# Performance work log

Hardware: AMD Instinct MI355X
Metric: run time of the kernel (lower is better)

The kernel has to match this reference:

```python
import jax, jax.numpy as jnp
import numpy as np

N, E = 50000, 800000
IN_C, HID, OUT_C, HEADS = 256, 32, 16, 8
NEG_SLOPE = 0.2


def gat_conv(x, edge_index, W, att_src, att_dst, bias, heads, out_c, concat):
    """PyG-style GATConv (inference, dropout off, add_self_loops=True).

    x: [N, F_in], edge_index: [2, E] with row0=src(j), row1=dst(i).
    W: [F_in, heads*out_c], att_src/att_dst: [heads, out_c], bias: [heads*out_c] or [out_c].
    """
    n = x.shape[0]
    loops = jnp.arange(n, dtype=edge_index.dtype)
    src = jnp.concatenate([edge_index[0], loops])
    dst = jnp.concatenate([edge_index[1], loops])

    xl = (x @ W).reshape(n, heads, out_c)              # [N, H, C]
    a_src = jnp.einsum('nhc,hc->nh', xl, att_src)      # [N, H]
    a_dst = jnp.einsum('nhc,hc->nh', xl, att_dst)

    e = a_src[src] + a_dst[dst]                        # [E', H]
    e = jnp.where(e >= 0, e, NEG_SLOPE * e)            # leaky_relu
    e_max = jax.ops.segment_max(e, dst, num_segments=n)
    e_exp = jnp.exp(e - e_max[dst])
    denom = jax.ops.segment_sum(e_exp, dst, num_segments=n)
    alpha = e_exp / (denom[dst] + 1e-16)               # segment softmax over in-edges of dst

    msg = alpha[:, :, None] * xl[src]                  # [E', H, C]
    out = jax.ops.segment_sum(msg, dst, num_segments=n)  # [N, H, C]
    if concat:
        out = out.reshape(n, heads * out_c)
    else:
        out = out.mean(axis=1)
    return out + bias


def setup_inputs() -> dict:
    key = jax.random.key(0)
    ks = jax.random.split(key, 10)
    s_in = 1.0 / np.sqrt(IN_C)
    s_h = 1.0 / np.sqrt(HEADS * HID)
    x = jax.random.normal(ks[0], (N, IN_C), dtype=jnp.float32)
    edge_index = jax.random.randint(ks[1], (2, E), 0, N, dtype=jnp.int64)
    return {
        'x': x,
        'edge_index': edge_index,
        'W1': jax.random.normal(ks[2], (IN_C, HEADS * HID), dtype=jnp.float32) * s_in,
        'att_src1': jax.random.normal(ks[3], (HEADS, HID), dtype=jnp.float32) * s_h,
        'att_dst1': jax.random.normal(ks[4], (HEADS, HID), dtype=jnp.float32) * s_h,
        'b1': jnp.zeros((HEADS * HID,), dtype=jnp.float32),
        'W2': jax.random.normal(ks[5], (HEADS * HID, OUT_C), dtype=jnp.float32) * s_h,
        'att_src2': jax.random.normal(ks[6], (1, OUT_C), dtype=jnp.float32) * 0.1,
        'att_dst2': jax.random.normal(ks[7], (1, OUT_C), dtype=jnp.float32) * 0.1,
        'b2': jnp.zeros((OUT_C,), dtype=jnp.float32),
    }


def reference(x, edge_index, W1, att_src1, att_dst1, b1, W2, att_src2, att_dst2, b2):
    h = gat_conv(x, edge_index, W1, att_src1, att_dst1, b1, HEADS, HID, concat=True)
    h = jax.nn.relu(h)
    # F.dropout(training=False) is identity at inference
    out = gat_conv(h, edge_index, W2, att_src2, att_dst2, b2, 1, OUT_C, concat=False)
    return jax.nn.log_softmax(out, axis=1)
```

## Files before the change

kernel.cpp:

```cpp
#include <hip/hip_runtime.h>

#define IN_C 256
#define H1 8
#define C1 32
#define F1 256
#define OC 16
#define NEG 0.2f

typedef short short8 __attribute__((ext_vector_type(8)));
typedef unsigned short ushort8 __attribute__((ext_vector_type(8)));
typedef float floatx4 __attribute__((ext_vector_type(4)));

__device__ __forceinline__ unsigned short f2bf(float f) {
    unsigned u = __builtin_bit_cast(unsigned, f);
    u = (u + 0x7fffu + ((u >> 16) & 1u)) >> 16;
    return (unsigned short)u;
}
__device__ __forceinline__ float bf2f(unsigned short h) {
    unsigned u = ((unsigned)h) << 16;
    return __builtin_bit_cast(float, u);
}

__global__ __launch_bounds__(256) void k_fuse0(const int* __restrict__ ei,
                                               int* __restrict__ cnt,
                                               const float* __restrict__ W1,
                                               const float* __restrict__ W2,
                                               unsigned short* __restrict__ w1t,
                                               unsigned short* __restrict__ w2t, int E)
{
    int gid = blockIdx.x * 256 + threadIdx.x;
    if (gid < E) atomicAdd(&cnt[ei[E + gid]], 1);
    if (gid < 65536) {
        int n = gid >> 8, k = gid & 255;
        w1t[n * 256 + k] = f2bf(W1[k * 256 + n]);
    } else if (gid < 65536 + 4096) {
        int r = gid - 65536;
        int n = r >> 8, k = r & 255;
        w2t[n * 256 + k] = f2bf(W2[k * 16 + n]);
    }
}

__global__ __launch_bounds__(256) void k_gemm1(const float* __restrict__ A,
                                               const unsigned short* __restrict__ Bt,
                                               const float* __restrict__ att_s,
                                               const float* __restrict__ att_d,
                                               unsigned short* __restrict__ Cb,
                                               float* __restrict__ asrc,
                                               float* __restrict__ adst, int M)
{
    __shared__ short As[128][40];
    __shared__ short Bs[128][40];
    const int tid  = threadIdx.x;
    const int lane = tid & 63;
    const int w    = tid >> 6;
    const int bm   = blockIdx.x * 128;
    const int bn   = blockIdx.y * 128;
    const int wm   = (w >> 1) * 64;
    const int wn   = (w & 1) * 64;
    const int srow = tid >> 1;
    const int soff = (tid & 1) * 16;
    floatx4 acc[4][4] = {};
    for (int k0 = 0; k0 < 256; k0 += 32) {
        __syncthreads();
        {
            int gr = bm + srow;
            float4 f0 = {0,0,0,0}, f1 = {0,0,0,0}, f2 = {0,0,0,0}, f3 = {0,0,0,0};
            if (gr < M) {
                const float4* p = (const float4*)(A + (size_t)gr * 256 + k0 + soff);
                f0 = p[0]; f1 = p[1]; f2 = p[2]; f3 = p[3];
            }
            ushort8 v0, v1;
            v0[0]=f2bf(f0.x); v0[1]=f2bf(f0.y); v0[2]=f2bf(f0.z); v0[3]=f2bf(f0.w);
            v0[4]=f2bf(f1.x); v0[5]=f2bf(f1.y); v0[6]=f2bf(f1.z); v0[7]=f2bf(f1.w);
            v1[0]=f2bf(f2.x); v1[1]=f2bf(f2.y); v1[2]=f2bf(f2.z); v1[3]=f2bf(f2.w);
            v1[4]=f2bf(f3.x); v1[5]=f2bf(f3.y); v1[6]=f2bf(f3.z); v1[7]=f2bf(f3.w);
            *(ushort8*)&As[srow][soff]     = v0;
            *(ushort8*)&As[srow][soff + 8] = v1;
        }
        {
            const ushort8* p = (const ushort8*)(Bt + (size_t)(bn + srow) * 256 + k0 + soff);
            *(ushort8*)&Bs[srow][soff]     = p[0];
            *(ushort8*)&Bs[srow][soff + 8] = p[1];
        }
        __syncthreads();
        short8 af[4], bf[4];
        const int q8 = (lane >> 4) * 8;
        const int l15i = lane & 15;
#pragma unroll
        for (int i = 0; i < 4; ++i) af[i] = *(const short8*)&As[wm + i * 16 + l15i][q8];
#pragma unroll
        for (int j = 0; j < 4; ++j) bf[j] = *(const short8*)&Bs[wn + j * 16 + l15i][q8];
#pragma unroll
        for (int i = 0; i < 4; ++i)
#pragma unroll
            for (int j = 0; j < 4; ++j)
                acc[i][j] = __builtin_amdgcn_mfma_f32_16x16x32_bf16(af[i], bf[j], acc[i][j], 0, 0, 0);
    }
    const int l15 = lane & 15;
    const int rq  = (lane >> 4) * 4;
    const int hA = (bn + wn) >> 5;
    const int hB = hA + 1;
    const float aS_A0 = att_s[hA * 32 + l15],      aS_A1 = att_s[hA * 32 + 16 + l15];
    const float aS_B0 = att_s[hB * 32 + l15],      aS_B1 = att_s[hB * 32 + 16 + l15];
    const float aD_A0 = att_d[hA * 32 + l15],      aD_A1 = att_d[hA * 32 + 16 + l15];
    const float aD_B0 = att_d[hB * 32 + l15],      aD_B1 = att_d[hB * 32 + 16 + l15];
#pragma unroll
    for (int i = 0; i < 4; ++i) {
#pragma unroll
        for (int reg = 0; reg < 4; ++reg) {
            int gr = bm + wm + i * 16 + rq + reg;
            float sA = acc[i][0][reg] * aS_A0 + acc[i][1][reg] * aS_A1;
            float dA = acc[i][0][reg] * aD_A0 + acc[i][1][reg] * aD_A1;
            float sB = acc[i][2][reg] * aS_B0 + acc[i][3][reg] * aS_B1;
            float dB = acc[i][2][reg] * aD_B0 + acc[i][3][reg] * aD_B1;
#pragma unroll
            for (int o = 1; o < 16; o <<= 1) {
                sA += __shfl_xor(sA, o, 16);  dA += __shfl_xor(dA, o, 16);
                sB += __shfl_xor(sB, o, 16);  dB += __shfl_xor(dB, o, 16);
            }
            if (gr < M) {
#pragma unroll
                for (int j = 0; j < 4; ++j)
                    Cb[(size_t)gr * 256 + bn + wn + j * 16 + l15] = f2bf(acc[i][j][reg]);
                if (l15 == 0) {
                    asrc[(size_t)gr * H1 + hA] = sA;  adst[(size_t)gr * H1 + hA] = dA;
                    asrc[(size_t)gr * H1 + hB] = sB;  adst[(size_t)gr * H1 + hB] = dB;
                }
            }
        }
    }
}

__global__ __launch_bounds__(256) void k_scan_a(const int* __restrict__ cnt,
                                                int* __restrict__ rp,
                                                int* __restrict__ bsum, int N)
{
    __shared__ int ws4[4];
    int t = threadIdx.x, lane = t & 63, wid = t >> 6;
    int i = blockIdx.x * 256 + t;
    int v = (i < N) ? cnt[i] : 0;
    int incl = v;
#pragma unroll
    for (int off = 1; off < 64; off <<= 1) {
        int tv = __shfl_up(incl, off, 64);
        if (lane >= off) incl += tv;
    }
    if (lane == 63) ws4[wid] = incl;
    __syncthreads();
    int add = 0;
    for (int w = 0; w < wid; ++w) add += ws4[w];
    incl += add;
    if (i < N) rp[i + 1] = incl;
    if (t == 255) bsum[blockIdx.x] = incl;
}

__global__ __launch_bounds__(256) void k_scan_b(const int* __restrict__ bsum,
                                                int* __restrict__ boff, int NB)
{
    __shared__ int ws4[4];
    int t = threadIdx.x, lane = t & 63, wid = t >> 6;
    int i0 = t * 4;
    int v[4];
#pragma unroll
    for (int k = 0; k < 4; ++k) { int i = i0 + k; v[k] = (i < NB) ? bsum[i] : 0; }
    int s = v[0] + v[1] + v[2] + v[3];
    int incl = s;
#pragma unroll
    for (int off = 1; off < 64; off <<= 1) {
        int tv = __shfl_up(incl, off, 64);
        if (lane >= off) incl += tv;
    }
    if (lane == 63) ws4[wid] = incl;
    __syncthreads();
    int wpre = 0;
    for (int w = 0; w < wid; ++w) wpre += ws4[w];
    int run = wpre + incl - s;
#pragma unroll
    for (int k = 0; k < 4; ++k) {
        int i = i0 + k;
        if (i < NB) boff[i] = run;
        run += v[k];
    }
}

__global__ __launch_bounds__(256) void k_scan_c(int* __restrict__ rp,
                                                const int* __restrict__ boff,
                                                const int* __restrict__ cnt,
                                                int* __restrict__ cur, int N)
{
    int i = blockIdx.x * 256 + threadIdx.x;
    if (i < N) {
        int v = rp[i + 1] + boff[blockIdx.x];
        rp[i + 1] = v;
        cur[i] = v - cnt[i];
    }
    if (i == 0) rp[0] = 0;
}

__global__ __launch_bounds__(256) void k_scatter(const int* __restrict__ ei,
                                                 int* __restrict__ cur,
                                                 int* __restrict__ ssrc, int E)
{
    int e = blockIdx.x * 256 + threadIdx.x;
    if (e >= E) return;
    int s = ei[e];
    int d = ei[E + e];
    int pos = atomicAdd(&cur[d], 1);
    ssrc[pos] = s;
}

__global__ __launch_bounds__(256) void k_gather1(const int* __restrict__ rp,
                                                 const int* __restrict__ ssrc,
                                                 const unsigned short* __restrict__ xl,
                                                 const float* __restrict__ asrc,
                                                 const float* __restrict__ adst,
                                                 const float* __restrict__ bias,
                                                 unsigned short* __restrict__ hout, int N)
{
    int lane = threadIdx.x & 63;
    int node = blockIdx.x * 4 + (threadIdx.x >> 6);
    if (node >= N) return;
    int half = lane >> 5;
    int l31  = lane & 31;
    int c8   = l31 * 8;
    int h    = l31 >> 2;
    float ad = adst[(size_t)node * H1 + h];

    float4 a0 = {0,0,0,0}, a1 = {0,0,0,0};
    float den = 0.f;

    if (half == 0) {
        float e = asrc[(size_t)node * H1 + h] + ad;
        e = e >= 0.f ? e : NEG * e;
        float w = __expf(e);
        ushort8 r = *(const ushort8*)(xl + (size_t)node * F1 + c8);
        a0.x += w*bf2f(r[0]); a0.y += w*bf2f(r[1]); a0.z += w*bf2f(r[2]); a0.w += w*bf2f(r[3]);
        a1.x += w*bf2f(r[4]); a1.y += w*bf2f(r[5]); a1.z += w*bf2f(r[6]); a1.w += w*bf2f(r[7]);
        den += w;
    }

    int jb = rp[node];
    int Ecnt = rp[node + 1] - jb;
    int k = half;
    for (; k + 2 < Ecnt; k += 4) {
        int s0 = ssrc[jb + k];
        int s1 = ssrc[jb + k + 2];
        float e0 = asrc[(size_t)s0 * H1 + h] + ad;
        float e1 = asrc[(size_t)s1 * H1 + h] + ad;
        ushort8 r0 = *(const ushort8*)(xl + (size_t)s0 * F1 + c8);
        ushort8 r1 = *(const ushort8*)(xl + (size_t)s1 * F1 + c8);
        e0 = e0 >= 0.f ? e0 : NEG * e0;  float w0 = __expf(e0);
        e1 = e1 >= 0.f ? e1 : NEG * e1;  float w1 = __expf(e1);
        den += w0 + w1;
        a0.x += w0*bf2f(r0[0]) + w1*bf2f(r1[0]);
        a0.y += w0*bf2f(r0[1]) + w1*bf2f(r1[1]);
        a0.z += w0*bf2f(r0[2]) + w1*bf2f(r1[2]);
        a0.w += w0*bf2f(r0[3]) + w1*bf2f(r1[3]);
        a1.x += w0*bf2f(r0[4]) + w1*bf2f(r1[4]);
        a1.y += w0*bf2f(r0[5]) + w1*bf2f(r1[5]);
        a1.z += w0*bf2f(r0[6]) + w1*bf2f(r1[6]);
        a1.w += w0*bf2f(r0[7]) + w1*bf2f(r1[7]);
    }
    if (k < Ecnt) {
        int s = ssrc[jb + k];
        float e = asrc[(size_t)s * H1 + h] + ad;
        e = e >= 0.f ? e : NEG * e;
        float w = __expf(e);
        ushort8 r = *(const ushort8*)(xl + (size_t)s * F1 + c8);
        den += w;
        a0.x += w*bf2f(r[0]); a0.y += w*bf2f(r[1]); a0.z += w*bf2f(r[2]); a0.w += w*bf2f(r[3]);
        a1.x += w*bf2f(r[4]); a1.y += w*bf2f(r[5]); a1.z += w*bf2f(r[6]); a1.w += w*bf2f(r[7]);
    }
    a0.x += __shfl_xor(a0.x, 32);  a0.y += __shfl_xor(a0.y, 32);
    a0.z += __shfl_xor(a0.z, 32);  a0.w += __shfl_xor(a0.w, 32);
    a1.x += __shfl_xor(a1.x, 32);  a1.y += __shfl_xor(a1.y, 32);
    a1.z += __shfl_xor(a1.z, 32);  a1.w += __shfl_xor(a1.w, 32);
    den  += __shfl_xor(den, 32);
    if (half == 0) {
        float inv = 1.f / (den + 1e-16f);
        const float4* bv = (const float4*)(bias + c8);
        float4 b0 = bv[0], b1 = bv[1];
        ushort8 o;
        o[0] = f2bf(fmaxf(a0.x * inv + b0.x, 0.f));
        o[1] = f2bf(fmaxf(a0.y * inv + b0.y, 0.f));
        o[2] = f2bf(fmaxf(a0.z * inv + b0.z, 0.f));
        o[3] = f2bf(fmaxf(a0.w * inv + b0.w, 0.f));
        o[4] = f2bf(fmaxf(a1.x * inv + b1.x, 0.f));
        o[5] = f2bf(fmaxf(a1.y * inv + b1.y, 0.f));
        o[6] = f2bf(fmaxf(a1.z * inv + b1.z, 0.f));
        o[7] = f2bf(fmaxf(a1.w * inv + b1.w, 0.f));
        *(ushort8*)(hout + (size_t)node * F1 + c8) = o;
    }
}

__global__ __launch_bounds__(256) void k_gemm2(const unsigned short* __restrict__ Hm,
                                               const unsigned short* __restrict__ W2t,
                                               const float* __restrict__ as2,
                                               const float* __restrict__ ad2,
                                               unsigned short* __restrict__ xl2b,
                                               float* __restrict__ asrc,
                                               float* __restrict__ adst, int N)
{
    const int lane = threadIdx.x & 63;
    const int wid  = threadIdx.x >> 6;
    const int rowbase = blockIdx.x * 64 + wid * 16;
    const int col = lane & 15;
    const int q8  = (lane >> 4) * 8;
    const int m   = rowbase + col;
    const bool mv = m < N;
    const unsigned short* arow = Hm + (size_t)m * 256 + q8;
    const unsigned short* brow = W2t + (size_t)col * 256 + q8;
    floatx4 acc = {0.f, 0.f, 0.f, 0.f};
#pragma unroll
    for (int t = 0; t < 8; ++t) {
        short8 af = {0,0,0,0,0,0,0,0};
        if (mv) af = *(const short8*)(arow + t * 32);
        short8 bf = *(const short8*)(brow + t * 32);
        acc = __builtin_amdgcn_mfma_f32_16x16x32_bf16(af, bf, acc, 0, 0, 0);
    }
    float s_as = as2[col], s_ad = ad2[col];
    const int rq = (lane >> 4) * 4;
#pragma unroll
    for (int reg = 0; reg < 4; ++reg) {
        int row = rowbase + rq + reg;
        float v = acc[reg];
        float s1 = v * s_as, s2 = v * s_ad;
#pragma unroll
        for (int o = 1; o < 16; o <<= 1) { s1 += __shfl_xor(s1, o, 16); s2 += __shfl_xor(s2, o, 16); }
        if (row < N) {
            xl2b[(size_t)row * OC + col] = f2bf(v);
            if (col == 0) { asrc[row] = s1; adst[row] = s2; }
        }
    }
}

__global__ __launch_bounds__(256) void k_gather2(const int* __restrict__ rp,
                                                 const int* __restrict__ ssrc,
                                                 const unsigned short* __restrict__ xl2b,
                                                 const float* __restrict__ asrc,
                                                 const float* __restrict__ adst,
                                                 const float* __restrict__ bias,
                                                 float* __restrict__ out, int N)
{
    int sub  = threadIdx.x & 15;
    int node = blockIdx.x * 16 + (threadIdx.x >> 4);
    if (node >= N) return;
    float ad = adst[node];
    float e = asrc[node] + ad;
    e = e >= 0.f ? e : NEG * e;
    float w = __expf(e);
    float acc = w * bf2f(xl2b[(size_t)node * OC + sub]);
    float den = w;
    int jb = rp[node], je = rp[node + 1];
    int j = jb;
    for (; j + 4 <= je; j += 4) {
        int s0 = ssrc[j], s1i = ssrc[j+1], s2i = ssrc[j+2], s3i = ssrc[j+3];
        float e0 = asrc[s0] + ad, e1 = asrc[s1i] + ad, e2 = asrc[s2i] + ad, e3 = asrc[s3i] + ad;
        float v0 = bf2f(xl2b[(size_t)s0 * OC + sub]);
        float v1 = bf2f(xl2b[(size_t)s1i * OC + sub]);
        float v2 = bf2f(xl2b[(size_t)s2i * OC + sub]);
        float v3 = bf2f(xl2b[(size_t)s3i * OC + sub]);
        e0 = e0 >= 0.f ? e0 : NEG * e0;  float w0 = __expf(e0);
        e1 = e1 >= 0.f ? e1 : NEG * e1;  float w1 = __expf(e1);
        e2 = e2 >= 0.f ? e2 : NEG * e2;  float w2 = __expf(e2);
        e3 = e3 >= 0.f ? e3 : NEG * e3;  float w3 = __expf(e3);
        den += w0 + w1 + w2 + w3;
        acc += w0 * v0 + w1 * v1 + w2 * v2 + w3 * v3;
    }
    for (; j < je; ++j) {
        int s = ssrc[j];
        float ev = asrc[s] + ad;
        ev = ev >= 0.f ? ev : NEG * ev;
        float wv = __expf(ev);
        acc += wv * bf2f(xl2b[(size_t)s * OC + sub]);
        den += wv;
    }
    float v = acc / (den + 1e-16f) + bias[sub];
    float m = v;
#pragma unroll
    for (int o = 1; o < 16; o <<= 1) m = fmaxf(m, __shfl_xor(m, o, 16));
    float ex = __expf(v - m);
    float ss = ex;
#pragma unroll
    for (int o = 1; o < 16; o <<= 1) ss += __shfl_xor(ss, o, 16);
    out[(size_t)node * OC + sub] = v - m - logf(ss);
}

extern "C" void kernel_launch(void* const* d_in, const int* in_sizes, int n_in,
                              void* d_out, int out_size, void* d_ws, size_t ws_size,
                              hipStream_t stream)
{
    const float* x   = (const float*)d_in[0];
    const int*   ei  = (const int*)d_in[1];
    const float* W1  = (const float*)d_in[2];
    const float* as1 = (const float*)d_in[3];
    const float* ad1 = (const float*)d_in[4];
    const float* b1  = (const float*)d_in[5];
    const float* W2  = (const float*)d_in[6];
    const float* as2 = (const float*)d_in[7];
    const float* ad2 = (const float*)d_in[8];
    const float* b2  = (const float*)d_in[9];
    float* out = (float*)d_out;

    const int N = in_sizes[0] / IN_C;
    const int E = in_sizes[1] / 2;
    const int NB = (N + 255) / 256;

    char* base = (char*)d_ws;
    unsigned short* xl1b = (unsigned short*)base;
    unsigned short* hb   = xl1b + (size_t)N * F1;
    unsigned short* w1t  = hb + (size_t)N * F1;
    unsigned short* w2t  = w1t + 256 * 256;
    unsigned short* xl2b = w2t + 16 * 256;
    float* asrc1 = (float*)(xl2b + (size_t)N * OC);
    float* adst1 = asrc1 + (size_t)N * H1;
    float* asrc2 = adst1 + (size_t)N * H1;
    float* adst2 = asrc2 + N;
    int*   rp    = (int*)(adst2 + N);
    int*   cnt   = rp + (N + 1);
    int*   cur   = cnt + N;
    int*   bsum  = cur + N;
    int*   boff  = bsum + 1024;
    int*   ssrc  = boff + 1024;

    hipMemsetAsync(cnt, 0, (size_t)N * sizeof(int), stream);
    k_fuse0<<<(E + 255) / 256, 256, 0, stream>>>(ei, cnt, W1, W2, w1t, w2t, E);
    k_scan_a<<<NB, 256, 0, stream>>>(cnt, rp, bsum, N);
    k_scan_b<<<1, 256, 0, stream>>>(bsum, boff, NB);
    k_scan_c<<<NB, 256, 0, stream>>>(rp, boff, cnt, cur, N);
    k_scatter<<<(E + 255) / 256, 256, 0, stream>>>(ei, cur, ssrc, E);

    k_gemm1<<<dim3((N + 127) / 128, 2), 256, 0, stream>>>(x, w1t, as1, ad1, xl1b, asrc1, adst1, N);
    k_gather1<<<(N + 3) / 4, 256, 0, stream>>>(rp, ssrc, xl1b, asrc1, adst1, b1, hb, N);

    k_gemm2<<<(N + 63) / 64, 256, 0, stream>>>(hb, w2t, as2, ad2, xl2b, asrc2, adst2, N);
    k_gather2<<<(N + 15) / 16, 256, 0, stream>>>(rp, ssrc, xl2b, asrc2, adst2, b2, out, N);
}
```

Measured before the change: 322.4 us.

## Fuse CSR build into one cooperative kernel and widen gemm1 to full output width

```diff
diff --git a/kernel.cpp b/kernel.cpp
--- a/kernel.cpp
+++ b/kernel.cpp
@@ -1,4 +1,7 @@
 #include <hip/hip_runtime.h>
+#include <hip/hip_cooperative_groups.h>
+
+namespace cg = cooperative_groups;
 
 #define IN_C 256
 #define H1 8
@@ -21,22 +24,90 @@
     return __builtin_bit_cast(float, u);
 }
 
-__global__ __launch_bounds__(256) void k_fuse0(const int* __restrict__ ei,
-                                               int* __restrict__ cnt,
-                                               const float* __restrict__ W1,
-                                               const float* __restrict__ W2,
-                                               unsigned short* __restrict__ w1t,
-                                               unsigned short* __restrict__ w2t, int E)
-{
-    int gid = blockIdx.x * 256 + threadIdx.x;
-    if (gid < E) atomicAdd(&cnt[ei[E + gid]], 1);
-    if (gid < 65536) {
-        int n = gid >> 8, k = gid & 255;
+__global__ __launch_bounds__(256) void k_csr(const int* __restrict__ ei,
+                                             const float* __restrict__ W1,
+                                             const float* __restrict__ W2,
+                                             unsigned short* __restrict__ w1t,
+                                             unsigned short* __restrict__ w2t,
+                                             int* __restrict__ cnt,
+                                             int* __restrict__ rp,
+                                             int* __restrict__ cur,
+                                             int* __restrict__ bsum,
+                                             int* __restrict__ boff,
+                                             int* __restrict__ ssrc,
+                                             int N, int E)
+{
+    cg::grid_group grid = cg::this_grid();
+    __shared__ int ws4[4];
+    const int tid  = threadIdx.x;
+    const int lane = tid & 63;
+    const int wid  = tid >> 6;
+    const int b    = blockIdx.x;
+    const int gt   = b * 256 + tid;
+    const int GT   = gridDim.x * 256;
+
+    for (int i = gt; i < N; i += GT) cnt[i] = 0;
+    {
+        int n = gt >> 8, k = gt & 255;
         w1t[n * 256 + k] = f2bf(W1[k * 256 + n]);
-    } else if (gid < 65536 + 4096) {
-        int r = gid - 65536;
-        int n = r >> 8, k = r & 255;
+    }
+    if (gt < 4096) {
+        int n = gt >> 8, k = gt & 255;
         w2t[n * 256 + k] = f2bf(W2[k * 16 + n]);
+    }
+    grid.sync();
+
+    for (int e = gt; e < E; e += GT) atomicAdd(&cnt[ei[E + e]], 1);
+    grid.sync();
+
+    {
+        int v = (gt < N) ? cnt[gt] : 0;
+        int incl = v;
+#pragma unroll
+        for (int off = 1; off < 64; off <<= 1) {
+            int tv = __shfl_up(incl, off, 64);
+            if (lane >= off) incl += tv;
+        }
+        if (lane == 63) ws4[wid] = incl;
+        __syncthreads();
+        int add = 0;
+        for (int w = 0; w < wid; ++w) add += ws4[w];
+        incl += add;
+        if (gt < N) rp[gt + 1] = incl;
+        if (tid == 255) bsum[b] = incl;
+    }
+    grid.sync();
+
+    if (b == 0) {
+        int v = bsum[tid];
+        int incl = v;
+#pragma unroll
+        for (int off = 1; off < 64; off <<= 1) {
+            int tv = __shfl_up(incl, off, 64);
+            if (lane >= off) incl += tv;
+        }
+        __syncthreads();
+        if (lane == 63) ws4[wid] = incl;
+        __syncthreads();
+        int add = 0;
+        for (int w = 0; w < wid; ++w) add += ws4[w];
+        boff[tid] = add + incl - v;
+    }
+    grid.sync();
+
+    if (gt < N) {
+        int v = rp[gt + 1] + boff[b];
+        rp[gt + 1] = v;
+        cur[gt] = v - cnt[gt];
+    }
+    if (gt == 0) rp[0] = 0;
+    grid.sync();
+
+    for (int e = gt; e < E; e += GT) {
+        int s = ei[e];
+        int d = ei[E + e];
+        int pos = atomicAdd(&cur[d], 1);
+        ssrc[pos] = s;
     }
 }
 
@@ -49,17 +120,17 @@
                                                float* __restrict__ adst, int M)
 {
     __shared__ short As[128][40];
-    __shared__ short Bs[128][40];
     const int tid  = threadIdx.x;
     const int lane = tid & 63;
     const int w    = tid >> 6;
     const int bm   = blockIdx.x * 128;
-    const int bn   = blockIdx.y * 128;
     const int wm   = (w >> 1) * 64;
-    const int wn   = (w & 1) * 64;
+    const int wn   = (w & 1) * 128;
     const int srow = tid >> 1;
     const int soff = (tid & 1) * 16;
-    floatx4 acc[4][4] = {};
+    const int q8   = (lane >> 4) * 8;
+    const int l15  = lane & 15;
+    floatx4 acc[4][8] = {};
     for (int k0 = 0; k0 < 256; k0 += 32) {
         __syncthreads();
         {
@@ -77,136 +148,53 @@
             *(ushort8*)&As[srow][soff]     = v0;
             *(ushort8*)&As[srow][soff + 8] = v1;
         }
-        {
-            const ushort8* p = (const ushort8*)(Bt + (size_t)(bn + srow) * 256 + k0 + soff);
-            *(ushort8*)&Bs[srow][soff]     = p[0];
-            *(ushort8*)&Bs[srow][soff + 8] = p[1];
-        }
         __syncthreads();
-        short8 af[4], bf[4];
-        const int q8 = (lane >> 4) * 8;
-        const int l15i = lane & 15;
-#pragma unroll
-        for (int i = 0; i < 4; ++i) af[i] = *(const short8*)&As[wm + i * 16 + l15i][q8];
-#pragma unroll
-        for (int j = 0; j < 4; ++j) bf[j] = *(const short8*)&Bs[wn + j * 16 + l15i][q8];
-#pragma unroll
-        for (int i = 0; i < 4; ++i)
-#pragma unroll
-            for (int j = 0; j < 4; ++j)
-                acc[i][j] = __builtin_amdgcn_mfma_f32_16x16x32_bf16(af[i], bf[j], acc[i][j], 0, 0, 0);
-    }
-    const int l15 = lane & 15;
+        short8 af[4];
+#pragma unroll
+        for (int i = 0; i < 4; ++i) af[i] = *(const short8*)&As[wm + i * 16 + l15][q8];
+#pragma unroll
+        for (int j = 0; j < 8; ++j) {
+            short8 bf = *(const short8*)(Bt + (size_t)(wn + j * 16 + l15) * 256 + k0 + q8);
+#pragma unroll
+            for (int i = 0; i < 4; ++i)
+                acc[i][j] = __builtin_amdgcn_mfma_f32_16x16x32_bf16(af[i], bf, acc[i][j], 0, 0, 0);
+        }
+    }
     const int rq  = (lane >> 4) * 4;
-    const int hA = (bn + wn) >> 5;
-    const int hB = hA + 1;
-    const float aS_A0 = att_s[hA * 32 + l15],      aS_A1 = att_s[hA * 32 + 16 + l15];
-    const float aS_B0 = att_s[hB * 32 + l15],      aS_B1 = att_s[hB * 32 + 16 + l15];
-    const float aD_A0 = att_d[hA * 32 + l15],      aD_A1 = att_d[hA * 32 + 16 + l15];
-    const float aD_B0 = att_d[hB * 32 + l15],      aD_B1 = att_d[hB * 32 + 16 + l15];
+    const int hb0 = wn >> 5;
+    float aS0[4], aS1[4], aD0[4], aD1[4];
+#pragma unroll
+    for (int hl = 0; hl < 4; ++hl) {
+        int hh = hb0 + hl;
+        aS0[hl] = att_s[hh * 32 + l15];  aS1[hl] = att_s[hh * 32 + 16 + l15];
+        aD0[hl] = att_d[hh * 32 + l15];  aD1[hl] = att_d[hh * 32 + 16 + l15];
+    }
 #pragma unroll
     for (int i = 0; i < 4; ++i) {
 #pragma unroll
         for (int reg = 0; reg < 4; ++reg) {
             int gr = bm + wm + i * 16 + rq + reg;
-            float sA = acc[i][0][reg] * aS_A0 + acc[i][1][reg] * aS_A1;
-            float dA = acc[i][0][reg] * aD_A0 + acc[i][1][reg] * aD_A1;
-            float sB = acc[i][2][reg] * aS_B0 + acc[i][3][reg] * aS_B1;
-            float dB = acc[i][2][reg] * aD_B0 + acc[i][3][reg] * aD_B1;
-#pragma unroll
-            for (int o = 1; o < 16; o <<= 1) {
-                sA += __shfl_xor(sA, o, 16);  dA += __shfl_xor(dA, o, 16);
-                sB += __shfl_xor(sB, o, 16);  dB += __shfl_xor(dB, o, 16);
+            if (gr < M) {
+#pragma unroll
+                for (int j = 0; j < 8; ++j)
+                    Cb[(size_t)gr * 256 + wn + j * 16 + l15] = f2bf(acc[i][j][reg]);
             }
-            if (gr < M) {
-#pragma unroll
-                for (int j = 0; j < 4; ++j)
-                    Cb[(size_t)gr * 256 + bn + wn + j * 16 + l15] = f2bf(acc[i][j][reg]);
-                if (l15 == 0) {
-                    asrc[(size_t)gr * H1 + hA] = sA;  adst[(size_t)gr * H1 + hA] = dA;
-                    asrc[(size_t)gr * H1 + hB] = sB;  adst[(size_t)gr * H1 + hB] = dB;
+#pragma unroll
+            for (int hl = 0; hl < 4; ++hl) {
+                float s = acc[i][2*hl][reg] * aS0[hl] + acc[i][2*hl+1][reg] * aS1[hl];
+                float d = acc[i][2*hl][reg] * aD0[hl] + acc[i][2*hl+1][reg] * aD1[hl];
+#pragma unroll
+                for (int o = 1; o < 16; o <<= 1) {
+                    s += __shfl_xor(s, o, 16);
+                    d += __shfl_xor(d, o, 16);
+                }
+                if (gr < M && l15 == 0) {
+                    asrc[(size_t)gr * H1 + hb0 + hl] = s;
+                    adst[(size_t)gr * H1 + hb0 + hl] = d;
                 }
             }
         }
     }
-}
-
-__global__ __launch_bounds__(256) void k_scan_a(const int* __restrict__ cnt,
-                                                int* __restrict__ rp,
-                                                int* __restrict__ bsum, int N)
-{
-    __shared__ int ws4[4];
-    int t = threadIdx.x, lane = t & 63, wid = t >> 6;
-    int i = blockIdx.x * 256 + t;
-    int v = (i < N) ? cnt[i] : 0;
-    int incl = v;
-#pragma unroll
-    for (int off = 1; off < 64; off <<= 1) {
-        int tv = __shfl_up(incl, off, 64);
-        if (lane >= off) incl += tv;
-    }
-    if (lane == 63) ws4[wid] = incl;
-    __syncthreads();
-    int add = 0;
-    for (int w = 0; w < wid; ++w) add += ws4[w];
-    incl += add;
-    if (i < N) rp[i + 1] = incl;
-    if (t == 255) bsum[blockIdx.x] = incl;
-}
-
-__global__ __launch_bounds__(256) void k_scan_b(const int* __restrict__ bsum,
-                                                int* __restrict__ boff, int NB)
-{
-    __shared__ int ws4[4];
-    int t = threadIdx.x, lane = t & 63, wid = t >> 6;
-    int i0 = t * 4;
-    int v[4];
-#pragma unroll
-    for (int k = 0; k < 4; ++k) { int i = i0 + k; v[k] = (i < NB) ? bsum[i] : 0; }
-    int s = v[0] + v[1] + v[2] + v[3];
-    int incl = s;
-#pragma unroll
-    for (int off = 1; off < 64; off <<= 1) {
-        int tv = __shfl_up(incl, off, 64);
-        if (lane >= off) incl += tv;
-    }
-    if (lane == 63) ws4[wid] = incl;
-    __syncthreads();
-    int wpre = 0;
-    for (int w = 0; w < wid; ++w) wpre += ws4[w];
-    int run = wpre + incl - s;
-#pragma unroll
-    for (int k = 0; k < 4; ++k) {
-        int i = i0 + k;
-        if (i < NB) boff[i] = run;
-        run += v[k];
-    }
-}
-
-__global__ __launch_bounds__(256) void k_scan_c(int* __restrict__ rp,
-                                                const int* __restrict__ boff,
-                                                const int* __restrict__ cnt,
-                                                int* __restrict__ cur, int N)
-{
-    int i = blockIdx.x * 256 + threadIdx.x;
-    if (i < N) {
-        int v = rp[i + 1] + boff[blockIdx.x];
-        rp[i + 1] = v;
-        cur[i] = v - cnt[i];
-    }
-    if (i == 0) rp[0] = 0;
-}
-
-__global__ __launch_bounds__(256) void k_scatter(const int* __restrict__ ei,
-                                                 int* __restrict__ cur,
-                                                 int* __restrict__ ssrc, int E)
-{
-    int e = blockIdx.x * 256 + threadIdx.x;
-    if (e >= E) return;
-    int s = ei[e];
-    int d = ei[E + e];
-    int pos = atomicAdd(&cur[d], 1);
-    ssrc[pos] = s;
 }
 
 __global__ __launch_bounds__(256) void k_gather1(const int* __restrict__ rp,
@@ -402,9 +390,8 @@
     const float* b2  = (const float*)d_in[9];
     float* out = (float*)d_out;
 
-    const int N = in_sizes[0] / IN_C;
-    const int E = in_sizes[1] / 2;
-    const int NB = (N + 255) / 256;
+    int N = in_sizes[0] / IN_C;
+    int E = in_sizes[1] / 2;
 
     char* base = (char*)d_ws;
     unsigned short* xl1b = (unsigned short*)base;
@@ -420,17 +407,17 @@
     int*   cnt   = rp + (N + 1);
     int*   cur   = cnt + N;
     int*   bsum  = cur + N;
-    int*   boff  = bsum + 1024;
-    int*   ssrc  = boff + 1024;
-
-    hipMemsetAsync(cnt, 0, (size_t)N * sizeof(int), stream);
-    k_fuse0<<<(E + 255) / 256, 256, 0, stream>>>(ei, cnt, W1, W2, w1t, w2t, E);
-    k_scan_a<<<NB, 256, 0, stream>>>(cnt, rp, bsum, N);
-    k_scan_b<<<1, 256, 0, stream>>>(bsum, boff, NB);
-    k_scan_c<<<NB, 256, 0, stream>>>(rp, boff, cnt, cur, N);
-    k_scatter<<<(E + 255) / 256, 256, 0, stream>>>(ei, cur, ssrc, E);
-
-    k_gemm1<<<dim3((N + 127) / 128, 2), 256, 0, stream>>>(x, w1t, as1, ad1, xl1b, asrc1, adst1, N);
+    int*   boff  = bsum + 256;
+    int*   ssrc  = boff + 256;
+
+    {
+        void* args[] = { (void*)&ei, (void*)&W1, (void*)&W2, (void*)&w1t, (void*)&w2t,
+                         (void*)&cnt, (void*)&rp, (void*)&cur, (void*)&bsum, (void*)&boff,
+                         (void*)&ssrc, (void*)&N, (void*)&E };
+        hipLaunchCooperativeKernel((void*)k_csr, dim3(256), dim3(256), args, 0, stream);
+    }
+
+    k_gemm1<<<(N + 127) / 128, 256, 0, stream>>>(x, w1t, as1, ad1, xl1b, asrc1, adst1, N);
     k_gather1<<<(N + 3) / 4, 256, 0, stream>>>(rp, ssrc, xl1b, asrc1, adst1, b1, hb, N);
 
     k_gemm2<<<(N + 63) / 64, 256, 0, stream>>>(hb, w2t, as2, ad2, xl2b, asrc2, adst2, N);
```

Measured after the change: 487.1 us. 51.1% more time.
